# Kernel optimization log

Measured on AMD Instinct MI355X. Metric: run time of the kernel, lower is better.

## Reference

```python
import jax, jax.numpy as jnp
import numpy as np

B, T, C, H = 4, 4096, 1024, 64

def setup_inputs() -> dict:
    key = jax.random.key(0)
    kx, kq, kk, kv = jax.random.split(key, 4)
    x  = jax.random.normal(kx, (B, T, C), dtype=jnp.float32)
    # nn.Linear(C, H, bias=False) weights have shape [H, C]; y = x @ W.T
    Wq = jax.random.normal(kq, (H, C), dtype=jnp.float32) * (C ** -0.5)
    Wk = jax.random.normal(kk, (H, C), dtype=jnp.float32) * (C ** -0.5)
    Wv = jax.random.normal(kv, (H, C), dtype=jnp.float32) * (C ** -0.5)
    return {"x": x, "Wq": Wq, "Wk": Wk, "Wv": Wv}

def reference(x, Wq, Wk, Wv):
    T_ = x.shape[1]
    scale = jnp.asarray(Wq.shape[0] ** -0.5, dtype=x.dtype)
    q = jnp.einsum('btc,hc->bth', x, Wq)
    k = jnp.einsum('btc,hc->bth', x, Wk)
    v = jnp.einsum('btc,hc->bth', x, Wv)
    w = jnp.einsum('bqh,bkh->bqk', q, k)  # [B, T, T] scores
    causal = jnp.tril(jnp.ones((T_, T_), dtype=bool))
    # original: masked_fill(-inf) then scale; -inf * scale == -inf, so equivalent
    w = jnp.where(causal, w * scale, -jnp.inf)
    w = jax.nn.softmax(w, axis=-1)
    # dropout p=0.0 (eval/deterministic): identity
    return jnp.einsum('bqk,bkh->bqh', w, v)
```

## Files before the change

### kernel.cpp

```cpp
#include <hip/hip_runtime.h>
#include <hip/hip_bf16.h>

#define B_ 4
#define T_ 4096
#define C_ 1024

typedef __bf16 bf16_t;
typedef __bf16 bf16x8 __attribute__((ext_vector_type(8)));
typedef float f32x4 __attribute__((ext_vector_type(4)));

__device__ __forceinline__ void gld16(const void* g, void* l) {
    __builtin_amdgcn_global_load_lds((const __attribute__((address_space(1))) void*)g,
                                     (__attribute__((address_space(3))) void*)l, 16, 0, 0);
}

__global__ void wcvt_kernel(const float* __restrict__ Wq, const float* __restrict__ Wk,
                            const float* __restrict__ Wv, bf16_t* __restrict__ wbf) {
    int i = blockIdx.x * 256 + threadIdx.x;
    int m = i >> 16;
    int r = i & 65535;
    const float* src = (m == 0) ? Wq : (m == 1) ? Wk : Wv;
    float s = (m == 0) ? 0.125f * 1.44269504f : 1.0f;
    wbf[i] = (bf16_t)(src[r] * s);
}

__global__ __launch_bounds__(512, 4)
void qkv_proj_kernel(const float* __restrict__ x, const bf16_t* __restrict__ wbf,
                     bf16_t* __restrict__ qb, bf16_t* __restrict__ kb,
                     bf16_t* __restrict__ vtb) {
    __shared__ float  xs[3][2048];
    __shared__ bf16_t wsb[2][12288];

    const int tid = threadIdx.x;
    const int w = tid >> 6, lane = tid & 63, lr = lane & 15, kg = lane >> 4;
    const int rg = w & 1, cg = w >> 1;
    const int row0 = blockIdx.x * 32;

    const int xr0 = tid >> 4, xu = tid & 15;
    const char* xg = (const char*)x + (size_t)(row0 + xr0) * 4096
                     + ((xu ^ (xr0 & 15)) * 16);
    const int wh = tid >> 3, wu = tid & 7;
    const char* wg = (const char*)wbf;

    char* xs_c  = (char*)&xs[0][0];
    char* xs_n  = (char*)&xs[1][0];
    char* xs_nn = (char*)&xs[2][0];
    char* ws_c  = (char*)&wsb[0][0];
    char* ws_n  = (char*)&wsb[1][0];

#define ISSUE_X(kk, dst) {                                                          \
        gld16(xg + (size_t)(kk) * 256, (dst) + (size_t)tid * 16); }
#define ISSUE_W(kk, dst) {                                                          \
        _Pragma("unroll")                                                           \
        for (int j = 0; j < 3; ++j) {                                               \
            int h = wh + j * 64;                                                    \
            gld16(wg + (size_t)h * 2048 + (size_t)(kk) * 128 + ((wu ^ (h & 7)) * 16), \
                  (dst) + (size_t)(tid + j * 512) * 16); } }

    f32x4 acc[3];
    #pragma unroll
    for (int j = 0; j < 3; ++j) acc[j] = (f32x4){0.f, 0.f, 0.f, 0.f};

    ISSUE_X(0, xs_c);
    ISSUE_W(0, ws_c);
    ISSUE_X(1, xs_n);

    const int rl = rg * 16 + lr;
    const int u00 = ((2 * kg)     ^ lr) * 16;
    const int u01 = ((2 * kg + 1) ^ lr) * 16;
    const int u10 = ((2 * kg + 8) ^ lr) * 16;
    const int u11 = ((2 * kg + 9) ^ lr) * 16;

    #pragma clang loop unroll(disable)
    for (int c = 0; c < 16; ++c) {
        if (c < 15) {
            asm volatile("s_waitcnt vmcnt(1)" ::: "memory");
        } else {
            asm volatile("s_waitcnt vmcnt(0)" ::: "memory");
        }
        __builtin_amdgcn_s_barrier();
        if (c < 15) ISSUE_W(c + 1, ws_n);
        if (c < 14) ISSUE_X(c + 2, xs_nn);

        {
            const char* xrow = xs_c + (size_t)rl * 256;
            float4 a0 = *(const float4*)(xrow + u00);
            float4 a1 = *(const float4*)(xrow + u01);
            float4 b0 = *(const float4*)(xrow + u10);
            float4 b1 = *(const float4*)(xrow + u11);
            bf16x8 af0, af1;
            af0[0]=(bf16_t)a0.x; af0[1]=(bf16_t)a0.y; af0[2]=(bf16_t)a0.z; af0[3]=(bf16_t)a0.w;
            af0[4]=(bf16_t)a1.x; af0[5]=(bf16_t)a1.y; af0[6]=(bf16_t)a1.z; af0[7]=(bf16_t)a1.w;
            af1[0]=(bf16_t)b0.x; af1[1]=(bf16_t)b0.y; af1[2]=(bf16_t)b0.z; af1[3]=(bf16_t)b0.w;
            af1[4]=(bf16_t)b1.x; af1[5]=(bf16_t)b1.y; af1[6]=(bf16_t)b1.z; af1[7]=(bf16_t)b1.w;

            __builtin_amdgcn_s_setprio(1);
            #pragma unroll
            for (int j = 0; j < 3; ++j) {
                int h = (cg * 3 + j) * 16 + lr;
                const char* wrow = ws_c + (size_t)h * 128;
                bf16x8 w0 = *(const bf16x8*)(wrow + (((kg)     ^ (lr & 7)) * 16));
                bf16x8 w1 = *(const bf16x8*)(wrow + (((kg + 4) ^ (lr & 7)) * 16));
                acc[j] = __builtin_amdgcn_mfma_f32_16x16x32_bf16(af0, w0, acc[j], 0, 0, 0);
                acc[j] = __builtin_amdgcn_mfma_f32_16x16x32_bf16(af1, w1, acc[j], 0, 0, 0);
            }
            __builtin_amdgcn_s_setprio(0);
        }

        char* tx = xs_c; xs_c = xs_n; xs_n = xs_nn; xs_nn = tx;
        char* tw = ws_c; ws_c = ws_n; ws_n = tw;
    }

    #pragma unroll
    for (int j = 0; j < 3; ++j) {
        int p = cg * 3 + j;
        int m = p >> 2;
        int h = (p & 3) * 16 + lr;
        #pragma unroll
        for (int i = 0; i < 4; ++i) {
            int t = row0 + rg * 16 + kg * 4 + i;
            float v = acc[j][i];
            if (m == 0) {
                qb[(size_t)t * 64 + h] = (bf16_t)v;
            } else if (m == 1) {
                kb[(size_t)t * 64 + ((((h >> 3) ^ (t & 7)) << 3) | (h & 7))] = (bf16_t)v;
            } else {
                int bb = t >> 12, tt = t & 4095;
                vtb[(size_t)(bb * 64 + h) * 4096 + (tt & ~63)
                    + (((((tt >> 3) & 7) ^ (h & 7))) << 3) + (tt & 7)] = (bf16_t)v;
            }
        }
    }
#undef ISSUE_X
#undef ISSUE_W
}

__global__ __launch_bounds__(256, 2)
void attn_kernel(const bf16_t* __restrict__ qb, const bf16_t* __restrict__ kb,
                 const bf16_t* __restrict__ vtb, float* __restrict__ po,
                 float* __restrict__ pl) {
    __shared__ bf16_t kvb[3][8192];
    __shared__ bf16_t p_lds[4][16][68];

    const int tid = threadIdx.x;
    const int w = tid >> 6, lane = tid & 63, lr = lane & 15, kg = lane >> 4;
    const int bid = blockIdx.x;
    const int b = bid & 3;
    const int v = bid >> 2;
    const int s = v & 3;
    const int qt = 63 - (v >> 2);
    const int qrow0 = qt * 64 + w * 16;
    const size_t bT = (size_t)b * 4096;

    const int nch   = qt + 1;
    const int start = (nch * s) >> 2;
    const int end   = (nch * (s + 1)) >> 2;
    const int cnt   = end - start;

    char* ks_c  = (char*)&kvb[0][0];
    char* ks_n  = (char*)&kvb[1][0];
    char* ks_nn = (char*)&kvb[2][0];

#define STAGE_CHUNK(kk, dst) {                                                      \
        _Pragma("unroll")                                                           \
        for (int jj = 0; jj < 2; ++jj) {                                            \
            int idx = tid + jj * 256;                                               \
            gld16((const char*)kb + (bT + (size_t)(kk) * 64) * 128 + (size_t)idx * 16, \
                  (dst) + (size_t)idx * 16);                                        \
            gld16((const char*)vtb + (size_t)(b * 64 + (idx >> 3)) * 8192           \
                      + (size_t)(kk) * 128 + (idx & 7) * 16,                        \
                  (dst) + 8192 + (size_t)idx * 16); } }

    bf16x8 qf[2];
    #pragma unroll
    for (int s2 = 0; s2 < 2; ++s2)
        qf[s2] = *(const bf16x8*)&qb[(bT + qrow0 + lr) * 64 + s2 * 32 + kg * 8];

    f32x4 o_acc[4];
    float l_i[4];
    #pragma unroll
    for (int ct = 0; ct < 4; ++ct) o_acc[ct] = (f32x4){0.f, 0.f, 0.f, 0.f};
    #pragma unroll
    for (int i = 0; i < 4; ++i) l_i[i] = 0.f;

    if (cnt > 0) STAGE_CHUNK(start, ks_c);
    if (cnt > 1) STAGE_CHUNK(start + 1, ks_n);

    for (int j = 0; j < cnt; ++j) {
        if (j < cnt - 1) {
            asm volatile("s_waitcnt vmcnt(4)" ::: "memory");
        } else {
            asm volatile("s_waitcnt vmcnt(0)" ::: "memory");
        }
        __builtin_amdgcn_s_barrier();
        asm volatile("" ::: "memory");
        if (j + 2 < cnt) STAGE_CHUNK(start + j + 2, ks_nn);

        const bf16_t* Kt = (const bf16_t*)ks_c;
        const bf16_t* Vt = (const bf16_t*)(ks_c + 8192);
        const int c = start + j;
        const int kv0 = c * 64;

        f32x4 sc[4];
        #pragma unroll
        for (int ct = 0; ct < 4; ++ct) sc[ct] = (f32x4){0.f, 0.f, 0.f, 0.f};
        __builtin_amdgcn_s_setprio(1);
        #pragma unroll
        for (int ct = 0; ct < 4; ++ct)
            #pragma unroll
            for (int s2 = 0; s2 < 2; ++s2) {
                bf16x8 kf = *(const bf16x8*)&Kt[(ct * 16 + lr) * 64 + (((kg + 4 * s2) ^ (lr & 7)) * 8)];
                sc[ct] = __builtin_amdgcn_mfma_f32_16x16x32_bf16(qf[s2], kf, sc[ct], 0, 0, 0);
            }
        __builtin_amdgcn_s_setprio(0);

        if (c == nch - 1) {
            #pragma unroll
            for (int ct = 0; ct < 4; ++ct)
                #pragma unroll
                for (int i = 0; i < 4; ++i) {
                    int col = kv0 + ct * 16 + lr;
                    int rw  = qrow0 + kg * 4 + i;
                    if (col > rw) sc[ct][i] = -INFINITY;
                }
        }

        #pragma unroll
        for (int ct = 0; ct < 4; ++ct)
            #pragma unroll
            for (int i = 0; i < 4; ++i) {
                float p = __builtin_amdgcn_exp2f(sc[ct][i]);
                p_lds[w][kg * 4 + i][ct * 16 + lr] = (bf16_t)p;
                l_i[i] += p;
            }

        bf16x8 pf[2];
        #pragma unroll
        for (int s2 = 0; s2 < 2; ++s2)
            pf[s2] = *(const bf16x8*)&p_lds[w][lr][s2 * 32 + kg * 8];
        __builtin_amdgcn_s_setprio(1);
        #pragma unroll
        for (int ct = 0; ct < 4; ++ct)
            #pragma unroll
            for (int s2 = 0; s2 < 2; ++s2) {
                bf16x8 vf = *(const bf16x8*)&Vt[(ct * 16 + lr) * 64 + (((kg + 4 * s2) ^ (lr & 7)) * 8)];
                o_acc[ct] = __builtin_amdgcn_mfma_f32_16x16x32_bf16(pf[s2], vf, o_acc[ct], 0, 0, 0);
            }
        __builtin_amdgcn_s_setprio(0);

        char* t0 = ks_c; ks_c = ks_n; ks_n = ks_nn; ks_nn = t0;
    }

    #pragma unroll
    for (int off = 1; off < 16; off <<= 1)
        #pragma unroll
        for (int i = 0; i < 4; ++i)
            l_i[i] += __shfl_xor(l_i[i], off);

    const size_t pbase = ((size_t)s * 4 + b) * 4096;
    #pragma unroll
    for (int i = 0; i < 4; ++i) {
        int row = qt * 64 + w * 16 + kg * 4 + i;
        #pragma unroll
        for (int ct = 0; ct < 4; ++ct)
            po[(pbase + row) * 64 + ct * 16 + lr] = o_acc[ct][i];
        if (lr == 0) pl[pbase + row] = l_i[i];
    }
#undef STAGE_CHUNK
}

__global__ __launch_bounds__(256)
void combine_kernel(const float* __restrict__ po, const float* __restrict__ pl,
                    float* __restrict__ out) {
    int idx = blockIdx.x * 256 + threadIdx.x;
    int row = idx >> 4;
    const f32x4* p4 = (const f32x4*)po;
    f32x4 vsum = p4[idx] + p4[262144 + idx] + p4[2 * 262144 + idx] + p4[3 * 262144 + idx];
    float l = pl[row] + pl[16384 + row] + pl[32768 + row] + pl[49152 + row];
    ((f32x4*)out)[idx] = vsum * (1.0f / l);
}

extern "C" void kernel_launch(void* const* d_in, const int* in_sizes, int n_in,
                              void* d_out, int out_size, void* d_ws, size_t ws_size,
                              hipStream_t stream) {
    const float* x  = (const float*)d_in[0];
    const float* Wq = (const float*)d_in[1];
    const float* Wk = (const float*)d_in[2];
    const float* Wv = (const float*)d_in[3];
    float* out = (float*)d_out;

    bf16_t* ws  = (bf16_t*)d_ws;
    bf16_t* wbf = ws;
    bf16_t* qb  = ws + 196608;
    bf16_t* kb  = qb + 1048576;
    bf16_t* vtb = kb + 1048576;
    float*  po  = (float*)(vtb + 1048576);
    float*  pl  = po + 4 * 1048576;

    wcvt_kernel<<<768, 256, 0, stream>>>(Wq, Wk, Wv, wbf);
    qkv_proj_kernel<<<512, 512, 0, stream>>>(x, wbf, qb, kb, vtb);
    attn_kernel<<<1024, 256, 0, stream>>>(qb, kb, vtb, po, pl);
    combine_kernel<<<1024, 256, 0, stream>>>(po, pl, out);
}
```

Before: 56.02 us.

## Double query rows per attention block to reuse staged K/V tiles

Each attention block now covers 128 query rows instead of 64: every wave handles two 16-row groups against each staged K/V chunk, and the grid is halved to 512 blocks. The aim is to halve the global-to-LDS traffic for K/V per query row and give each wave more MFMA work per chunk. The causal mask is now applied per row group wherever a chunk crosses the diagonal. In exchange, register pressure goes up, there are fewer blocks to fill the CUs, and per-block work along the causal triangle is less even.

```diff
diff --git a/kernel.cpp b/kernel.cpp
--- a/kernel.cpp
+++ b/kernel.cpp
@@ -140,7 +140,7 @@
                  const bf16_t* __restrict__ vtb, float* __restrict__ po,
                  float* __restrict__ pl) {
     __shared__ bf16_t kvb[3][8192];
-    __shared__ bf16_t p_lds[4][16][68];
+    __shared__ bf16_t p_lds[4][32][68];
 
     const int tid = threadIdx.x;
     const int w = tid >> 6, lane = tid & 63, lr = lane & 15, kg = lane >> 4;
@@ -148,11 +148,11 @@
     const int b = bid & 3;
     const int v = bid >> 2;
     const int s = v & 3;
-    const int qt = 63 - (v >> 2);
-    const int qrow0 = qt * 64 + w * 16;
+    const int qt = 31 - (v >> 2);
+    const int qrow0 = qt * 128 + w * 32;
     const size_t bT = (size_t)b * 4096;
 
-    const int nch   = qt + 1;
+    const int nch   = 2 * (qt + 1);
     const int start = (nch * s) >> 2;
     const int end   = (nch * (s + 1)) >> 2;
     const int cnt   = end - start;
@@ -171,17 +171,25 @@
                       + (size_t)(kk) * 128 + (idx & 7) * 16,                        \
                   (dst) + 8192 + (size_t)idx * 16); } }
 
-    bf16x8 qf[2];
-    #pragma unroll
-    for (int s2 = 0; s2 < 2; ++s2)
-        qf[s2] = *(const bf16x8*)&qb[(bT + qrow0 + lr) * 64 + s2 * 32 + kg * 8];
-
-    f32x4 o_acc[4];
-    float l_i[4];
-    #pragma unroll
-    for (int ct = 0; ct < 4; ++ct) o_acc[ct] = (f32x4){0.f, 0.f, 0.f, 0.f};
-    #pragma unroll
-    for (int i = 0; i < 4; ++i) l_i[i] = 0.f;
+    bf16x8 qf[2][2];
+    #pragma unroll
+    for (int rg = 0; rg < 2; ++rg)
+        #pragma unroll
+        for (int s2 = 0; s2 < 2; ++s2)
+            qf[rg][s2] = *(const bf16x8*)&qb[(bT + qrow0 + rg * 16 + lr) * 64 + s2 * 32 + kg * 8];
+
+    f32x4 o_acc[2][4];
+    float l_i[2][4];
+    #pragma unroll
+    for (int rg = 0; rg < 2; ++rg)
+        #pragma unroll
+        for (int ct = 0; ct < 4; ++ct) {
+            o_acc[rg][ct] = (f32x4){0.f, 0.f, 0.f, 0.f};
+        }
+    #pragma unroll
+    for (int rg = 0; rg < 2; ++rg)
+        #pragma unroll
+        for (int i = 0; i < 4; ++i) l_i[rg][i] = 0.f;
 
     if (cnt > 0) STAGE_CHUNK(start, ks_c);
     if (cnt > 1) STAGE_CHUNK(start + 1, ks_n);
@@ -198,53 +206,63 @@
 
         const bf16_t* Kt = (const bf16_t*)ks_c;
         const bf16_t* Vt = (const bf16_t*)(ks_c + 8192);
-        const int c = start + j;
-        const int kv0 = c * 64;
-
-        f32x4 sc[4];
-        #pragma unroll
-        for (int ct = 0; ct < 4; ++ct) sc[ct] = (f32x4){0.f, 0.f, 0.f, 0.f};
+        const int kv0 = (start + j) * 64;
+
+        f32x4 sc[2][4];
+        #pragma unroll
+        for (int rg = 0; rg < 2; ++rg)
+            #pragma unroll
+            for (int ct = 0; ct < 4; ++ct) sc[rg][ct] = (f32x4){0.f, 0.f, 0.f, 0.f};
         __builtin_amdgcn_s_setprio(1);
         #pragma unroll
         for (int ct = 0; ct < 4; ++ct)
             #pragma unroll
             for (int s2 = 0; s2 < 2; ++s2) {
                 bf16x8 kf = *(const bf16x8*)&Kt[(ct * 16 + lr) * 64 + (((kg + 4 * s2) ^ (lr & 7)) * 8)];
-                sc[ct] = __builtin_amdgcn_mfma_f32_16x16x32_bf16(qf[s2], kf, sc[ct], 0, 0, 0);
+                sc[0][ct] = __builtin_amdgcn_mfma_f32_16x16x32_bf16(qf[0][s2], kf, sc[0][ct], 0, 0, 0);
+                sc[1][ct] = __builtin_amdgcn_mfma_f32_16x16x32_bf16(qf[1][s2], kf, sc[1][ct], 0, 0, 0);
             }
         __builtin_amdgcn_s_setprio(0);
 
-        if (c == nch - 1) {
+        #pragma unroll
+        for (int rg = 0; rg < 2; ++rg) {
+            if (kv0 + 63 > qrow0 + rg * 16) {
+                #pragma unroll
+                for (int ct = 0; ct < 4; ++ct)
+                    #pragma unroll
+                    for (int i = 0; i < 4; ++i) {
+                        int col = kv0 + ct * 16 + lr;
+                        int rw  = qrow0 + rg * 16 + kg * 4 + i;
+                        if (col > rw) sc[rg][ct][i] = -INFINITY;
+                    }
+            }
+        }
+
+        #pragma unroll
+        for (int rg = 0; rg < 2; ++rg)
             #pragma unroll
             for (int ct = 0; ct < 4; ++ct)
                 #pragma unroll
                 for (int i = 0; i < 4; ++i) {
-                    int col = kv0 + ct * 16 + lr;
-                    int rw  = qrow0 + kg * 4 + i;
-                    if (col > rw) sc[ct][i] = -INFINITY;
+                    float p = __builtin_amdgcn_exp2f(sc[rg][ct][i]);
+                    p_lds[w][rg * 16 + kg * 4 + i][ct * 16 + lr] = (bf16_t)p;
+                    l_i[rg][i] += p;
                 }
-        }
-
-        #pragma unroll
-        for (int ct = 0; ct < 4; ++ct)
-            #pragma unroll
-            for (int i = 0; i < 4; ++i) {
-                float p = __builtin_amdgcn_exp2f(sc[ct][i]);
-                p_lds[w][kg * 4 + i][ct * 16 + lr] = (bf16_t)p;
-                l_i[i] += p;
-            }
-
-        bf16x8 pf[2];
-        #pragma unroll
-        for (int s2 = 0; s2 < 2; ++s2)
-            pf[s2] = *(const bf16x8*)&p_lds[w][lr][s2 * 32 + kg * 8];
+
+        bf16x8 pf[2][2];
+        #pragma unroll
+        for (int rg = 0; rg < 2; ++rg)
+            #pragma unroll
+            for (int s2 = 0; s2 < 2; ++s2)
+                pf[rg][s2] = *(const bf16x8*)&p_lds[w][rg * 16 + lr][s2 * 32 + kg * 8];
         __builtin_amdgcn_s_setprio(1);
         #pragma unroll
         for (int ct = 0; ct < 4; ++ct)
             #pragma unroll
             for (int s2 = 0; s2 < 2; ++s2) {
                 bf16x8 vf = *(const bf16x8*)&Vt[(ct * 16 + lr) * 64 + (((kg + 4 * s2) ^ (lr & 7)) * 8)];
-                o_acc[ct] = __builtin_amdgcn_mfma_f32_16x16x32_bf16(pf[s2], vf, o_acc[ct], 0, 0, 0);
+                o_acc[0][ct] = __builtin_amdgcn_mfma_f32_16x16x32_bf16(pf[0][s2], vf, o_acc[0][ct], 0, 0, 0);
+                o_acc[1][ct] = __builtin_amdgcn_mfma_f32_16x16x32_bf16(pf[1][s2], vf, o_acc[1][ct], 0, 0, 0);
             }
         __builtin_amdgcn_s_setprio(0);
 
@@ -254,18 +272,22 @@
     #pragma unroll
     for (int off = 1; off < 16; off <<= 1)
         #pragma unroll
-        for (int i = 0; i < 4; ++i)
-            l_i[i] += __shfl_xor(l_i[i], off);
+        for (int rg = 0; rg < 2; ++rg)
+            #pragma unroll
+            for (int i = 0; i < 4; ++i)
+                l_i[rg][i] += __shfl_xor(l_i[rg][i], off);
 
     const size_t pbase = ((size_t)s * 4 + b) * 4096;
     #pragma unroll
-    for (int i = 0; i < 4; ++i) {
-        int row = qt * 64 + w * 16 + kg * 4 + i;
-        #pragma unroll
-        for (int ct = 0; ct < 4; ++ct)
-            po[(pbase + row) * 64 + ct * 16 + lr] = o_acc[ct][i];
-        if (lr == 0) pl[pbase + row] = l_i[i];
-    }
+    for (int rg = 0; rg < 2; ++rg)
+        #pragma unroll
+        for (int i = 0; i < 4; ++i) {
+            int row = qt * 128 + w * 32 + rg * 16 + kg * 4 + i;
+            #pragma unroll
+            for (int ct = 0; ct < 4; ++ct)
+                po[(pbase + row) * 64 + ct * 16 + lr] = o_acc[rg][ct][i];
+            if (lr == 0) pl[pbase + row] = l_i[rg][i];
+        }
 #undef STAGE_CHUNK
 }
 
@@ -299,6 +321,6 @@
 
     wcvt_kernel<<<768, 256, 0, stream>>>(Wq, Wk, Wv, wbf);
     qkv_proj_kernel<<<512, 512, 0, stream>>>(x, wbf, qb, kb, vtb);
-    attn_kernel<<<1024, 256, 0, stream>>>(qb, kb, vtb, po, pl);
+    attn_kernel<<<512, 256, 0, stream>>>(qb, kb, vtb, po, pl);
     combine_kernel<<<1024, 256, 0, stream>>>(po, pl, out);
 }
```

New measurement: 60.27 us. 7.6% more time.
